# Kernel optimization log

Hardware: AMD Instinct MI355X
Metric: run time of the kernel (lower is better)

The kernel has to match this reference:

```python
import jax, jax.numpy as jnp
import numpy as np

IMG = 128          # img_wh
K = 10             # points_per_pixel
RADIUS = 0.005     # rasterization radius in NDC units
BIG = 1e10         # sentinel depth for pixels a point does not cover


def setup_inputs() -> dict:
    key = jax.random.key(0)
    k1, k2 = jax.random.split(key)
    B, P = 2, 2048
    # points near origin; camera at t=(0,0,2) looking down +z -> z_cam ~ 2
    points = jax.random.normal(k1, (B, P, 3), jnp.float32) * 0.4
    features = jax.random.uniform(k2, (B, P, 3), jnp.float32)  # RGB per point
    cam_R = jnp.broadcast_to(jnp.eye(3, dtype=jnp.float32), (B, 3, 3))
    cam_t = jnp.broadcast_to(jnp.array([0.0, 0.0, 2.0], jnp.float32), (B, 3))
    f = jnp.array(128.0, jnp.float32)  # focal length in pixels (in_ndc=False)
    return {"points": points, "features": features, "cam_R": cam_R,
            "cam_t": cam_t, "f": f}


def _render(points, features, cam_R, cam_t, f):
    B, P, _ = points.shape
    # PyTorch3D extrinsics: x_cam = x_world @ R + T (row vectors)
    cam = jnp.einsum('bpi,bij->bpj', points, cam_R) + cam_t[:, None, :]
    x, y, z = cam[..., 0], cam[..., 1], cam[..., 2]
    cx = cy = IMG / 2.0
    # perspective projection to pixel coords (screen-space camera).
    # NDC axis flips used by PyTorch3D cancel inside the squared distance,
    # so distances (the only thing rasterization uses) are convention-free.
    px = f * x / z + cx  # [B,P]
    py = f * y / z + cy
    pix = jnp.arange(IMG, dtype=jnp.float32) + 0.5  # pixel centers
    gy, gx = jnp.meshgrid(pix, pix, indexing='ij')  # [H,W]
    gx = gx.reshape(-1)  # [HW]
    gy = gy.reshape(-1)
    scale = 2.0 / IMG  # pixels -> NDC units (square image)
    dx = (px[:, None, :] - gx[None, :, None]) * scale  # [B,HW,P]
    dy = (py[:, None, :] - gy[None, :, None]) * scale
    dist2 = dx * dx + dy * dy                           # [B,HW,P]
    hit = (dist2 < RADIUS * RADIUS) & (z[:, None, :] > 1e-3)
    zm = jnp.where(hit, z[:, None, :], BIG)             # masked depth
    # z-buffer: K nearest covering points per pixel (ascending depth)
    neg_top, idx = jax.lax.top_k(-zm, K)                # [B,HW,K]
    zbuf = -neg_top
    valid = zbuf < BIG * 0.5
    d2k = jnp.take_along_axis(dist2, idx, axis=-1)      # [B,HW,K]
    # PointsRenderer weights: 1 - dist2/r^2, clamped to [0,1]
    alpha = jnp.where(valid, jnp.clip(1.0 - d2k / (RADIUS * RADIUS), 0.0, 1.0), 0.0)
    b_idx = jnp.arange(B)[:, None, None]
    featk = features[b_idx, idx]                        # [B,HW,K,C]
    # front-to-back alpha compositing: w_k = a_k * prod_{j<k}(1-a_j)
    one_m = 1.0 - alpha
    T = jnp.concatenate([jnp.ones_like(alpha[..., :1]),
                         jnp.cumprod(one_m, axis=-1)[..., :-1]], axis=-1)
    w = alpha * T
    images = jnp.einsum('bnk,bnkc->bnc', w, featk).reshape(B, IMG, IMG, -1)
    # depth image = nearest z, background = -1 (PyTorch3D convention)
    depth = jnp.where(valid[..., 0], zbuf[..., 0], -1.0).reshape(B, IMG, IMG)
    return images, depth


def reference(points, features, cam_R, cam_t, f):
    return _render(points, features, cam_R, cam_t, f)
```

## Files before the change

kernel.cpp:

```cpp
#include <hip/hip_runtime.h>


constexpr int   IMGC  = 128;
constexpr int   HWC   = IMGC * IMGC;
constexpr int   KTOP  = 10;
constexpr int   CAP   = 16;
constexpr float BIGF  = 1e10f;
constexpr float R2C   = 2.5e-05f;
constexpr float SCALE = 0.015625f;

__global__ void zero_counts_kernel(int* __restrict__ counts, int n)
{
    int i = blockIdx.x * blockDim.x + threadIdx.x;
    if (i < n) counts[i] = 0;
}

__global__ void proj_scatter_kernel(const float* __restrict__ points,
                                    const float* __restrict__ camR,
                                    const float* __restrict__ camT,
                                    const float* __restrict__ fptr,
                                    float4* __restrict__ proj,
                                    int* __restrict__ counts,
                                    int* __restrict__ lists,
                                    int B, int P)
{
    int i = blockIdx.x * blockDim.x + threadIdx.x;
    if (i >= B * P) return;
    int b = i / P;
    int p = i - b * P;

    float p0 = points[3*i], p1 = points[3*i+1], p2 = points[3*i+2];
    const float* R = camR + 9*b;
    const float* t = camT + 3*b;
    float x = p0*R[0] + p1*R[3] + p2*R[6] + t[0];
    float y = p0*R[1] + p1*R[4] + p2*R[7] + t[1];
    float z = p0*R[2] + p1*R[5] + p2*R[8] + t[2];
    float f = fptr[0];
    float px = __fadd_rn(__fdiv_rn(__fmul_rn(f, x), z), 64.0f);
    float py = __fadd_rn(__fdiv_rn(__fmul_rn(f, y), z), 64.0f);
    proj[i] = make_float4(px, py, z, 0.0f);

    float fx = floorf(px), fy = floorf(py);
    if (!(fx >= 0.0f && fx <= 127.0f && fy >= 0.0f && fy <= 127.0f)) return;
    int col = (int)fx, row = (int)fy;
    float gx = col + 0.5f, gy = row + 0.5f;
    float dx = __fmul_rn(__fsub_rn(px, gx), SCALE);
    float dy = __fmul_rn(__fsub_rn(py, gy), SCALE);
    float d2 = __fadd_rn(__fmul_rn(dx, dx), __fmul_rn(dy, dy));
    if (d2 < R2C && z > 1e-3f) {
        int pixel = b * HWC + row * IMGC + col;
        int slot  = atomicAdd(&counts[pixel], 1);
        if (slot < CAP) lists[(size_t)pixel * CAP + slot] = p;
    }
}

__global__ void composite_kernel(const float4* __restrict__ proj,
                                 const int* __restrict__ counts,
                                 const int* __restrict__ lists,
                                 const float* __restrict__ feats,
                                 float* __restrict__ out,
                                 int B, int P)
{
    int t = blockIdx.x * blockDim.x + threadIdx.x;
    if (t >= B * HWC) return;
    int b   = t / HWC;
    int pix = t - b * HWC;

    int cnt = counts[t];
    if (cnt > CAP) cnt = CAP;

    float c0 = 0.0f, c1 = 0.0f, c2 = 0.0f, T = 1.0f, depth = -1.0f;
    if (cnt > 0) {
        int row = pix >> 7, col = pix & 127;
        float gx = col + 0.5f, gy = row + 0.5f;
        float prevz = -1e30f; int previ = -1;
        for (int k = 0; k < KTOP; ++k) {
            float bz = BIGF, bd2 = 0.0f; int bi = 0x7fffffff; bool found = false;
            for (int j = 0; j < cnt; ++j) {
                int pidx = lists[(size_t)t * CAP + j];
                float4 v = proj[(size_t)b * P + pidx];
                bool after = (v.z > prevz) || (v.z == prevz && pidx > previ);
                bool better = (v.z < bz) || (v.z == bz && pidx < bi);
                if (after && better) {
                    bz = v.z; bi = pidx;
                    float dx = __fmul_rn(__fsub_rn(v.x, gx), SCALE);
                    float dy = __fmul_rn(__fsub_rn(v.y, gy), SCALE);
                    bd2 = __fadd_rn(__fmul_rn(dx, dx), __fmul_rn(dy, dy));
                    found = true;
                }
            }
            if (!found) break;
            if (k == 0) depth = bz;
            float a = 1.0f - bd2 / R2C;
            a = fminf(fmaxf(a, 0.0f), 1.0f);
            float w = a * T;
            const float* ft = feats + ((size_t)b * P + bi) * 3;
            c0 += w * ft[0]; c1 += w * ft[1]; c2 += w * ft[2];
            T *= (1.0f - a);
            prevz = bz; previ = bi;
        }
    }

    float* img = out + (size_t)t * 3;
    img[0] = c0; img[1] = c1; img[2] = c2;
    out[(size_t)B * HWC * 3 + t] = depth;
}


__global__ void proj_kernel(const float* __restrict__ points,
                            const float* __restrict__ camR,
                            const float* __restrict__ camT,
                            const float* __restrict__ fptr,
                            float4* __restrict__ proj,
                            int B, int P)
{
    int i = blockIdx.x * blockDim.x + threadIdx.x;
    if (i >= B * P) return;
    int b = i / P;
    float p0 = points[3*i], p1 = points[3*i+1], p2 = points[3*i+2];
    const float* R = camR + 9*b;
    const float* t = camT + 3*b;
    float x = p0*R[0] + p1*R[3] + p2*R[6] + t[0];
    float y = p0*R[1] + p1*R[4] + p2*R[7] + t[1];
    float z = p0*R[2] + p1*R[5] + p2*R[8] + t[2];
    float f = fptr[0];
    float px = __fadd_rn(__fdiv_rn(__fmul_rn(f, x), z), 64.0f);
    float py = __fadd_rn(__fdiv_rn(__fmul_rn(f, y), z), 64.0f);
    proj[i] = make_float4(px, py, z, 0.0f);
}

__launch_bounds__(64)
__global__ void raster_kernel(const float4* __restrict__ proj,
                              const float* __restrict__ feats,
                              float* __restrict__ out,
                              int B, int P)
{
    __shared__ float4 sp[2048];
    const int blocks_per_b = HWC / 64;
    const int b   = blockIdx.x / blocks_per_b;
    const int pix = (blockIdx.x % blocks_per_b) * 64 + threadIdx.x;

    for (int i = threadIdx.x; i < P; i += 64)
        sp[i] = proj[b * P + i];
    __syncthreads();

    const int row = pix >> 7, col = pix & 127;
    const float gx = col + 0.5f, gy = row + 0.5f;

    float zk[KTOP], d2k[KTOP];
    int   ik[KTOP];
#pragma unroll
    for (int j = 0; j < KTOP; ++j) { zk[j] = BIGF; d2k[j] = 0.0f; ik[j] = 0; }

    for (int p = 0; p < P; ++p) {
        float4 v = sp[p];
        float dx = __fmul_rn(__fsub_rn(v.x, gx), SCALE);
        float dy = __fmul_rn(__fsub_rn(v.y, gy), SCALE);
        float d2 = __fadd_rn(__fmul_rn(dx, dx), __fmul_rn(dy, dy));
        bool hit = (d2 < R2C) && (v.z > 1e-3f);
        if (hit && v.z < zk[KTOP-1]) {
            zk[KTOP-1] = v.z; d2k[KTOP-1] = d2; ik[KTOP-1] = p;
#pragma unroll
            for (int j = KTOP-1; j > 0; --j) {
                if (zk[j] < zk[j-1]) {
                    float tz = zk[j];  zk[j]  = zk[j-1];  zk[j-1]  = tz;
                    float td = d2k[j]; d2k[j] = d2k[j-1]; d2k[j-1] = td;
                    int   ti = ik[j];  ik[j]  = ik[j-1];  ik[j-1]  = ti;
                }
            }
        }
    }

    float T = 1.0f, c0 = 0.0f, c1 = 0.0f, c2 = 0.0f;
#pragma unroll
    for (int j = 0; j < KTOP; ++j) {
        if (zk[j] < 0.5f * BIGF) {
            float a = 1.0f - d2k[j] / R2C;
            a = fminf(fmaxf(a, 0.0f), 1.0f);
            float w = a * T;
            const float* ft = feats + ((size_t)b * P + ik[j]) * 3;
            c0 += w * ft[0]; c1 += w * ft[1]; c2 += w * ft[2];
            T *= (1.0f - a);
        }
    }

    float* img = out + (size_t)(b * HWC + pix) * 3;
    img[0] = c0; img[1] = c1; img[2] = c2;
    out[(size_t)B * HWC * 3 + (size_t)b * HWC + pix] =
        (zk[0] < 0.5f * BIGF) ? zk[0] : -1.0f;
}

extern "C" void kernel_launch(void* const* d_in, const int* in_sizes, int n_in,
                              void* d_out, int out_size, void* d_ws, size_t ws_size,
                              hipStream_t stream) {
    const float* points = (const float*)d_in[0];
    const float* feats  = (const float*)d_in[1];
    const float* camR   = (const float*)d_in[2];
    const float* camT   = (const float*)d_in[3];
    const float* fptr   = (const float*)d_in[4];

    const int B = in_sizes[3] / 3;
    const int P = in_sizes[0] / (3 * B);
    const int np = B * P;
    const int npix = B * HWC;

    size_t off_proj   = 0;
    size_t off_counts = off_proj + (size_t)np * sizeof(float4);
    size_t off_lists  = off_counts + (size_t)npix * sizeof(int);
    size_t needed     = off_lists + (size_t)npix * CAP * sizeof(int);

    float* out = (float*)d_out;
    float4* proj = (float4*)((char*)d_ws + off_proj);

    if (ws_size >= needed) {
        int* counts = (int*)((char*)d_ws + off_counts);
        int* lists  = (int*)((char*)d_ws + off_lists);
        zero_counts_kernel<<<(npix + 255) / 256, 256, 0, stream>>>(counts, npix);
        proj_scatter_kernel<<<(np + 255) / 256, 256, 0, stream>>>(
            points, camR, camT, fptr, proj, counts, lists, B, P);
        composite_kernel<<<(npix + 255) / 256, 256, 0, stream>>>(
            proj, counts, lists, feats, out, B, P);
    } else {
        proj_kernel<<<(np + 255) / 256, 256, 0, stream>>>(points, camR, camT, fptr, proj, B, P);
        raster_kernel<<<B * HWC / 64, 64, 0, stream>>>(proj, feats, out, B, P);
    }
}
```

Measured before the change: 69.78 us.

## Fuse zero, scatter and composite into one cooperative kernel with precomputed list entries

Replaces the three-launch zero/scatter/composite pipeline with a single cooperative kernel that uses grid-wide syncs between phases. It also stores z, d2 and the point index directly in per-pixel list entries, so compositing no longer gathers from a projection buffer. The repeated-selection top-K is replaced with a single-pass insertion sort. This removes launch overhead and indirect loads, but adds grid-sync cost, quadruples list storage, and depends on all 128 blocks being co-resident; the old brute-force fallback is removed and the fallback path now needs the larger workspace.

```diff
diff --git a/kernel.cpp b/kernel.cpp
--- a/kernel.cpp
+++ b/kernel.cpp
@@ -1,4 +1,7 @@
 #include <hip/hip_runtime.h>
+#include <hip/hip_cooperative_groups.h>
+
+namespace cg = cooperative_groups;
 
 
 constexpr int   IMGC  = 128;
@@ -9,6 +12,106 @@
 constexpr float R2C   = 2.5e-05f;
 constexpr float SCALE = 0.015625f;
 
+__launch_bounds__(256)
+__global__ void fused_coop_kernel(const float* __restrict__ points,
+                                  const float* __restrict__ feats,
+                                  const float* __restrict__ camR,
+                                  const float* __restrict__ camT,
+                                  const float* __restrict__ fptr,
+                                  int* __restrict__ counts,
+                                  float4* __restrict__ lists,
+                                  float* __restrict__ out,
+                                  int B, int P)
+{
+    cg::grid_group grid = cg::this_grid();
+    const int tid  = blockIdx.x * blockDim.x + threadIdx.x;
+    const int npix = B * HWC;
+
+    if (tid < npix) counts[tid] = 0;
+    grid.sync();
+
+    if (tid < B * P) {
+        const int b = tid / P;
+        const int p = tid - b * P;
+        const float* pp = points + (size_t)tid * 3;
+        float p0 = pp[0], p1 = pp[1], p2 = pp[2];
+        const float* R = camR + 9 * b;
+        const float* t = camT + 3 * b;
+        float x = p0*R[0] + p1*R[3] + p2*R[6] + t[0];
+        float y = p0*R[1] + p1*R[4] + p2*R[7] + t[1];
+        float z = p0*R[2] + p1*R[5] + p2*R[8] + t[2];
+        float f = fptr[0];
+        float px = __fadd_rn(__fdiv_rn(__fmul_rn(f, x), z), 64.0f);
+        float py = __fadd_rn(__fdiv_rn(__fmul_rn(f, y), z), 64.0f);
+        float fx = floorf(px), fy = floorf(py);
+        if (fx >= 0.0f && fx <= 127.0f && fy >= 0.0f && fy <= 127.0f) {
+            int col = (int)fx, row = (int)fy;
+            float gx = col + 0.5f, gy = row + 0.5f;
+            float dx = __fmul_rn(__fsub_rn(px, gx), SCALE);
+            float dy = __fmul_rn(__fsub_rn(py, gy), SCALE);
+            float d2 = __fadd_rn(__fmul_rn(dx, dx), __fmul_rn(dy, dy));
+            if (d2 < R2C && z > 1e-3f) {
+                int pixel = b * HWC + row * IMGC + col;
+                int slot  = atomicAdd(&counts[pixel], 1);
+                if (slot < CAP)
+                    lists[(size_t)pixel * CAP + slot] =
+                        make_float4(z, d2, __int_as_float(p), 0.0f);
+            }
+        }
+    }
+    grid.sync();
+
+    if (tid < npix) {
+        const int b = tid / HWC;
+        int cnt = __hip_atomic_load(&counts[tid], __ATOMIC_RELAXED,
+                                    __HIP_MEMORY_SCOPE_AGENT);
+        if (cnt > CAP) cnt = CAP;
+
+        float zk[KTOP], d2k[KTOP];
+        int   ik[KTOP];
+#pragma unroll
+        for (int j = 0; j < KTOP; ++j) { zk[j] = BIGF; d2k[j] = 0.0f; ik[j] = 0x7fffffff; }
+
+        for (int j = 0; j < cnt; ++j) {
+            float4 v = lists[(size_t)tid * CAP + j];
+            float vz = v.x;
+            int   pi = __float_as_int(v.z);
+            if (vz < zk[KTOP-1] || (vz == zk[KTOP-1] && pi < ik[KTOP-1])) {
+                zk[KTOP-1] = vz; d2k[KTOP-1] = v.y; ik[KTOP-1] = pi;
+#pragma unroll
+                for (int q = KTOP-1; q > 0; --q) {
+                    bool sw = (zk[q] < zk[q-1]) ||
+                              (zk[q] == zk[q-1] && ik[q] < ik[q-1]);
+                    if (sw) {
+                        float tz = zk[q];  zk[q]  = zk[q-1];  zk[q-1]  = tz;
+                        float td = d2k[q]; d2k[q] = d2k[q-1]; d2k[q-1] = td;
+                        int   ti = ik[q];  ik[q]  = ik[q-1];  ik[q-1]  = ti;
+                    }
+                }
+            }
+        }
+
+        float T = 1.0f, c0 = 0.0f, c1 = 0.0f, c2 = 0.0f;
+#pragma unroll
+        for (int j = 0; j < KTOP; ++j) {
+            if (zk[j] < 0.5f * BIGF) {
+                float a = 1.0f - d2k[j] / R2C;
+                a = fminf(fmaxf(a, 0.0f), 1.0f);
+                float w = a * T;
+                const float* ft = feats + ((size_t)b * P + ik[j]) * 3;
+                c0 += w * ft[0]; c1 += w * ft[1]; c2 += w * ft[2];
+                T *= (1.0f - a);
+            }
+        }
+
+        float* img = out + (size_t)tid * 3;
+        img[0] = c0; img[1] = c1; img[2] = c2;
+        out[(size_t)B * HWC * 3 + tid] =
+            (zk[0] < 0.5f * BIGF) ? zk[0] : -1.0f;
+    }
+}
+
+
 __global__ void zero_counts_kernel(int* __restrict__ counts, int n)
 {
     int i = blockIdx.x * blockDim.x + threadIdx.x;
@@ -19,16 +122,14 @@
                                     const float* __restrict__ camR,
                                     const float* __restrict__ camT,
                                     const float* __restrict__ fptr,
-                                    float4* __restrict__ proj,
                                     int* __restrict__ counts,
-                                    int* __restrict__ lists,
+                                    float4* __restrict__ lists,
                                     int B, int P)
 {
     int i = blockIdx.x * blockDim.x + threadIdx.x;
     if (i >= B * P) return;
     int b = i / P;
     int p = i - b * P;
-
     float p0 = points[3*i], p1 = points[3*i+1], p2 = points[3*i+2];
     const float* R = camR + 9*b;
     const float* t = camT + 3*b;
@@ -38,8 +139,6 @@
     float f = fptr[0];
     float px = __fadd_rn(__fdiv_rn(__fmul_rn(f, x), z), 64.0f);
     float py = __fadd_rn(__fdiv_rn(__fmul_rn(f, y), z), 64.0f);
-    proj[i] = make_float4(px, py, z, 0.0f);
-
     float fx = floorf(px), fy = floorf(py);
     if (!(fx >= 0.0f && fx <= 127.0f && fy >= 0.0f && fy <= 127.0f)) return;
     int col = (int)fx, row = (int)fy;
@@ -50,122 +149,42 @@
     if (d2 < R2C && z > 1e-3f) {
         int pixel = b * HWC + row * IMGC + col;
         int slot  = atomicAdd(&counts[pixel], 1);
-        if (slot < CAP) lists[(size_t)pixel * CAP + slot] = p;
-    }
-}
-
-__global__ void composite_kernel(const float4* __restrict__ proj,
-                                 const int* __restrict__ counts,
-                                 const int* __restrict__ lists,
+        if (slot < CAP)
+            lists[(size_t)pixel * CAP + slot] = make_float4(z, d2, __int_as_float(p), 0.0f);
+    }
+}
+
+__global__ void composite_kernel(const int* __restrict__ counts,
+                                 const float4* __restrict__ lists,
                                  const float* __restrict__ feats,
                                  float* __restrict__ out,
                                  int B, int P)
 {
     int t = blockIdx.x * blockDim.x + threadIdx.x;
     if (t >= B * HWC) return;
-    int b   = t / HWC;
-    int pix = t - b * HWC;
-
+    int b = t / HWC;
     int cnt = counts[t];
     if (cnt > CAP) cnt = CAP;
 
-    float c0 = 0.0f, c1 = 0.0f, c2 = 0.0f, T = 1.0f, depth = -1.0f;
-    if (cnt > 0) {
-        int row = pix >> 7, col = pix & 127;
-        float gx = col + 0.5f, gy = row + 0.5f;
-        float prevz = -1e30f; int previ = -1;
-        for (int k = 0; k < KTOP; ++k) {
-            float bz = BIGF, bd2 = 0.0f; int bi = 0x7fffffff; bool found = false;
-            for (int j = 0; j < cnt; ++j) {
-                int pidx = lists[(size_t)t * CAP + j];
-                float4 v = proj[(size_t)b * P + pidx];
-                bool after = (v.z > prevz) || (v.z == prevz && pidx > previ);
-                bool better = (v.z < bz) || (v.z == bz && pidx < bi);
-                if (after && better) {
-                    bz = v.z; bi = pidx;
-                    float dx = __fmul_rn(__fsub_rn(v.x, gx), SCALE);
-                    float dy = __fmul_rn(__fsub_rn(v.y, gy), SCALE);
-                    bd2 = __fadd_rn(__fmul_rn(dx, dx), __fmul_rn(dy, dy));
-                    found = true;
-                }
-            }
-            if (!found) break;
-            if (k == 0) depth = bz;
-            float a = 1.0f - bd2 / R2C;
-            a = fminf(fmaxf(a, 0.0f), 1.0f);
-            float w = a * T;
-            const float* ft = feats + ((size_t)b * P + bi) * 3;
-            c0 += w * ft[0]; c1 += w * ft[1]; c2 += w * ft[2];
-            T *= (1.0f - a);
-            prevz = bz; previ = bi;
-        }
-    }
-
-    float* img = out + (size_t)t * 3;
-    img[0] = c0; img[1] = c1; img[2] = c2;
-    out[(size_t)B * HWC * 3 + t] = depth;
-}
-
-
-__global__ void proj_kernel(const float* __restrict__ points,
-                            const float* __restrict__ camR,
-                            const float* __restrict__ camT,
-                            const float* __restrict__ fptr,
-                            float4* __restrict__ proj,
-                            int B, int P)
-{
-    int i = blockIdx.x * blockDim.x + threadIdx.x;
-    if (i >= B * P) return;
-    int b = i / P;
-    float p0 = points[3*i], p1 = points[3*i+1], p2 = points[3*i+2];
-    const float* R = camR + 9*b;
-    const float* t = camT + 3*b;
-    float x = p0*R[0] + p1*R[3] + p2*R[6] + t[0];
-    float y = p0*R[1] + p1*R[4] + p2*R[7] + t[1];
-    float z = p0*R[2] + p1*R[5] + p2*R[8] + t[2];
-    float f = fptr[0];
-    float px = __fadd_rn(__fdiv_rn(__fmul_rn(f, x), z), 64.0f);
-    float py = __fadd_rn(__fdiv_rn(__fmul_rn(f, y), z), 64.0f);
-    proj[i] = make_float4(px, py, z, 0.0f);
-}
-
-__launch_bounds__(64)
-__global__ void raster_kernel(const float4* __restrict__ proj,
-                              const float* __restrict__ feats,
-                              float* __restrict__ out,
-                              int B, int P)
-{
-    __shared__ float4 sp[2048];
-    const int blocks_per_b = HWC / 64;
-    const int b   = blockIdx.x / blocks_per_b;
-    const int pix = (blockIdx.x % blocks_per_b) * 64 + threadIdx.x;
-
-    for (int i = threadIdx.x; i < P; i += 64)
-        sp[i] = proj[b * P + i];
-    __syncthreads();
-
-    const int row = pix >> 7, col = pix & 127;
-    const float gx = col + 0.5f, gy = row + 0.5f;
-
     float zk[KTOP], d2k[KTOP];
     int   ik[KTOP];
 #pragma unroll
-    for (int j = 0; j < KTOP; ++j) { zk[j] = BIGF; d2k[j] = 0.0f; ik[j] = 0; }
-
-    for (int p = 0; p < P; ++p) {
-        float4 v = sp[p];
-        float dx = __fmul_rn(__fsub_rn(v.x, gx), SCALE);
-        float dy = __fmul_rn(__fsub_rn(v.y, gy), SCALE);
-        float d2 = __fadd_rn(__fmul_rn(dx, dx), __fmul_rn(dy, dy));
-        bool hit = (d2 < R2C) && (v.z > 1e-3f);
-        if (hit && v.z < zk[KTOP-1]) {
-            zk[KTOP-1] = v.z; d2k[KTOP-1] = d2; ik[KTOP-1] = p;
-#pragma unroll
-            for (int j = KTOP-1; j > 0; --j) {
-                if (zk[j] < zk[j-1]) {
-                    float tz = zk[j];  zk[j]  = zk[j-1];  zk[j-1]  = tz;
-                    float td = d2k[j]; d2k[j] = d2k[j-1]; d2k[j-1] = td;
-                    int   ti = ik[j];  ik[j]  = ik[j-1];  ik[j-1]  = ti;
+    for (int j = 0; j < KTOP; ++j) { zk[j] = BIGF; d2k[j] = 0.0f; ik[j] = 0x7fffffff; }
+
+    for (int j = 0; j < cnt; ++j) {
+        float4 v = lists[(size_t)t * CAP + j];
+        float vz = v.x;
+        int   pi = __float_as_int(v.z);
+        if (vz < zk[KTOP-1] || (vz == zk[KTOP-1] && pi < ik[KTOP-1])) {
+            zk[KTOP-1] = vz; d2k[KTOP-1] = v.y; ik[KTOP-1] = pi;
+#pragma unroll
+            for (int q = KTOP-1; q > 0; --q) {
+                bool sw = (zk[q] < zk[q-1]) ||
+                          (zk[q] == zk[q-1] && ik[q] < ik[q-1]);
+                if (sw) {
+                    float tz = zk[q];  zk[q]  = zk[q-1];  zk[q-1]  = tz;
+                    float td = d2k[q]; d2k[q] = d2k[q-1]; d2k[q-1] = td;
+                    int   ti = ik[q];  ik[q]  = ik[q-1];  ik[q-1]  = ti;
                 }
             }
         }
@@ -184,10 +203,9 @@
         }
     }
 
-    float* img = out + (size_t)(b * HWC + pix) * 3;
+    float* img = out + (size_t)t * 3;
     img[0] = c0; img[1] = c1; img[2] = c2;
-    out[(size_t)B * HWC * 3 + (size_t)b * HWC + pix] =
-        (zk[0] < 0.5f * BIGF) ? zk[0] : -1.0f;
+    out[(size_t)B * HWC * 3 + t] = (zk[0] < 0.5f * BIGF) ? zk[0] : -1.0f;
 }
 
 extern "C" void kernel_launch(void* const* d_in, const int* in_sizes, int n_in,
@@ -199,29 +217,30 @@
     const float* camT   = (const float*)d_in[3];
     const float* fptr   = (const float*)d_in[4];
 
-    const int B = in_sizes[3] / 3;
-    const int P = in_sizes[0] / (3 * B);
-    const int np = B * P;
+    int B = in_sizes[3] / 3;
+    int P = in_sizes[0] / (3 * B);
+    const int np   = B * P;
     const int npix = B * HWC;
 
-    size_t off_proj   = 0;
-    size_t off_counts = off_proj + (size_t)np * sizeof(float4);
-    size_t off_lists  = off_counts + (size_t)npix * sizeof(int);
-    size_t needed     = off_lists + (size_t)npix * CAP * sizeof(int);
-
-    float* out = (float*)d_out;
-    float4* proj = (float4*)((char*)d_ws + off_proj);
+    size_t off_counts = 0;
+    size_t off_lists  = (off_counts + (size_t)npix * sizeof(int) + 255) & ~(size_t)255;
+    size_t needed     = off_lists + (size_t)npix * CAP * sizeof(float4);
+
+    int*    counts = (int*)((char*)d_ws + off_counts);
+    float4* lists  = (float4*)((char*)d_ws + off_lists);
+    float*  out    = (float*)d_out;
 
     if (ws_size >= needed) {
-        int* counts = (int*)((char*)d_ws + off_counts);
-        int* lists  = (int*)((char*)d_ws + off_lists);
+        void* args[] = {(void*)&points, (void*)&feats, (void*)&camR, (void*)&camT,
+                        (void*)&fptr, (void*)&counts, (void*)&lists, (void*)&out,
+                        (void*)&B, (void*)&P};
+        hipLaunchCooperativeKernel((const void*)fused_coop_kernel,
+                                   dim3(npix / 256), dim3(256), args, 0, stream);
+    } else {
         zero_counts_kernel<<<(npix + 255) / 256, 256, 0, stream>>>(counts, npix);
         proj_scatter_kernel<<<(np + 255) / 256, 256, 0, stream>>>(
-            points, camR, camT, fptr, proj, counts, lists, B, P);
+            points, camR, camT, fptr, counts, lists, B, P);
         composite_kernel<<<(npix + 255) / 256, 256, 0, stream>>>(
-            proj, counts, lists, feats, out, B, P);
-    } else {
-        proj_kernel<<<(np + 255) / 256, 256, 0, stream>>>(points, camR, camT, fptr, proj, B, P);
-        raster_kernel<<<B * HWC / 64, 64, 0, stream>>>(proj, feats, out, B, P);
-    }
-}
+            counts, lists, feats, out, B, P);
+    }
+}
```

New measurement: 112.6 us. 1.61x slower.
